# Kernel tuning notes

Hardware: AMD Instinct MI355X
Metric: run time of the kernel (lower is better)

The kernel has to match this reference:

```python
import jax, jax.numpy as jnp
import numpy as np

N_NODES = 50000
N_EDGES = 640000
D_IN = 128
D_H = 128


def gcn_conv(x, edge_index_sl, W, b, n_nodes):
    # x: [N, d_in]; edge_index_sl: [2, E+N] (self-loops already appended)
    h = x @ W  # [N, d_out]
    row, col = edge_index_sl[0], edge_index_sl[1]
    deg = jax.ops.segment_sum(jnp.ones(row.shape[0], dtype=x.dtype), col,
                              num_segments=n_nodes)
    dis = jnp.where(deg > 0, jax.lax.rsqrt(jnp.maximum(deg, 1e-12)), 0.0)
    norm = dis[row] * dis[col]  # [E+N]
    msg = h[row] * norm[:, None]  # gather + scale, [E+N, d_out]
    out = jax.ops.segment_sum(msg, col, num_segments=n_nodes)  # scatter-add
    return out + b


def setup_inputs() -> dict:
    key = jax.random.key(0)
    ks = jax.random.split(key, 9)
    x = jax.random.normal(ks[0], (N_NODES, D_IN), dtype=jnp.float32)
    edge_index = jax.random.randint(ks[1], (2, N_EDGES), 0, N_NODES, dtype=jnp.int64)
    s0 = 1.0 / np.sqrt(D_IN)
    s1 = 1.0 / np.sqrt(D_H)
    W0 = jax.random.uniform(ks[2], (D_IN, D_H), jnp.float32, -s0, s0)
    b0 = jnp.zeros((D_H,), jnp.float32)
    W1 = jax.random.uniform(ks[3], (D_H, D_H), jnp.float32, -s1, s1)
    b1 = jnp.zeros((D_H,), jnp.float32)
    W2 = jax.random.uniform(ks[4], (D_H, D_H), jnp.float32, -s1, s1)
    b2 = jnp.zeros((D_H,), jnp.float32)
    return {"x": x, "edge_index": edge_index, "W0": W0, "b0": b0,
            "W1": W1, "b1": b1, "W2": W2, "b2": b2}


def reference(x, edge_index, W0, b0, W1, b1, W2, b2):
    n = x.shape[0]
    # GCNConv adds self-loops: append (i, i) for every node.
    loops = jnp.arange(n, dtype=edge_index.dtype)
    ei = jnp.concatenate([edge_index, jnp.stack([loops, loops])], axis=1)
    h = x
    for W, b in ((W0, b0), (W1, b1), (W2, b2)):
        h = gcn_conv(h, ei, W, b, n)
        h = jax.nn.relu(h)  # dropout is identity in eval mode
    return h
```

## Files before the change

kernel.cpp:

```cpp
#include <hip/hip_runtime.h>
#include <hip/hip_bf16.h>

#define D 128
#define CAP 64
typedef _Float16 f16;
typedef unsigned short u16;
typedef f16 f16x8 __attribute__((ext_vector_type(8)));
typedef f16 f16x2 __attribute__((ext_vector_type(2)));
typedef float f32x4 __attribute__((ext_vector_type(4)));



__global__ void scatter_cvt_kernel(const int* __restrict__ row, const int* __restrict__ col,
                                   int* __restrict__ fill, u16* __restrict__ ssrc, int E,
                                   const float* __restrict__ W0, const float* __restrict__ W1,
                                   const float* __restrict__ W2,
                                   const float* __restrict__ b0, const float* __restrict__ b1,
                                   const float* __restrict__ b2,
                                   f16* __restrict__ WT, float* __restrict__ bperm) {
    const int EB = (E + 255) >> 8;
    const int b = blockIdx.x;
    if (b < EB) {
        int i = b * 256 + threadIdx.x;
        if (i < E) {
            int d = col[i];
            int p = atomicAdd(&fill[d], 1);
            if (p < CAP) ssrc[(size_t)d * CAP + p] = (u16)row[i];
        }
    } else {
        int id = (b - EB) * 256 + threadIdx.x;
        if (id < 49152) {
            int l = id >> 14;
            int e = id & 16383;
            int j = e >> 7;
            int nn = e & 127;
            int k = (l == 0) ? j : ((j >> 3) + 16 * (j & 7));
            const float* W = (l == 0) ? W0 : (l == 1) ? W1 : W2;
            WT[(size_t)l * 16384 + nn * 128 + j] = (f16)W[k * 128 + nn];
        } else if (id < 49536) {
            int j = id - 49152;
            int l = j >> 7;
            int pos = j & 127;
            int c = 16 * (pos & 7) + (pos >> 3);
            const float* bb = (l == 0) ? b0 : (l == 1) ? b1 : b2;
            bperm[l * 128 + pos] = bb[c];
        }
    }
}


template <bool A_F32>
__global__ __launch_bounds__(256) void gemm_mfma(const void* __restrict__ Aptr,
                                                 const f16* __restrict__ WT,
                                                 const int* __restrict__ fill,
                                                 f16* __restrict__ H, int n) {
    __shared__ f16 sW[128 * 128];
    const int tid  = threadIdx.x;
    const int w    = tid >> 6, lane = tid & 63;
    const int q    = lane >> 4, c = lane & 15;
    const int row0 = blockIdx.x * 64;

    int arow = row0 + w * 16 + c;
    if (arow >= n) arow = n - 1;

    f16x8 afr[4];
    if (A_F32) {
        float4 x0[4], x1[4];
        #pragma unroll
        for (int t = 0; t < 4; ++t) {
            const float* src = (const float*)Aptr + (size_t)arow * D + (t * 4 + q) * 8;
            x0[t] = *(const float4*)src;
            x1[t] = *(const float4*)(src + 4);
        }
        #pragma unroll
        for (int t = 0; t < 4; ++t) {
            f16x8 h;
            h[0] = (f16)x0[t].x; h[1] = (f16)x0[t].y; h[2] = (f16)x0[t].z; h[3] = (f16)x0[t].w;
            h[4] = (f16)x1[t].x; h[5] = (f16)x1[t].y; h[6] = (f16)x1[t].z; h[7] = (f16)x1[t].w;
            afr[t] = h;
        }
    } else {
        #pragma unroll
        for (int t = 0; t < 4; ++t)
            afr[t] = *(const f16x8*)((const f16*)Aptr + (size_t)arow * D + (t * 4 + q) * 8);
    }

    #pragma unroll
    for (int i = 0; i < 8; ++i) {
        int f = i * 256 + tid;
        int r = f >> 4, b = f & 15;
        int u = (r << 4) | (b ^ (r & 15));
        *(f16x8*)&sW[u * 8] = *(const f16x8*)&WT[(size_t)r * D + b * 8];
    }
    __syncthreads();

    f32x4 acc[8];
    #pragma unroll
    for (int nt = 0; nt < 8; ++nt) acc[nt] = (f32x4)0.f;

    #pragma unroll
    for (int nt = 0; nt < 8; ++nt) {
        const int rn = nt * 16 + c;
        #pragma unroll
        for (int t = 0; t < 4; ++t) {
            f16x8 bfr = *(const f16x8*)&sW[(((rn << 4) | ((t * 4 + q) ^ c))) * 8];
            acc[nt] = __builtin_amdgcn_mfma_f32_16x16x32_f16(afr[t], bfr, acc[nt], 0, 0, 0);
        }
    }

    const int rbase = row0 + w * 16 + q * 4;
    int4 fv4 = *(const int4*)&fill[rbase];
    #pragma unroll
    for (int reg = 0; reg < 4; ++reg) {
        int grow = rbase + reg;
        if (grow < n) {
            int fv = (reg == 0) ? fv4.x : (reg == 1) ? fv4.y : (reg == 2) ? fv4.z : fv4.w;
            float dv = rsqrtf((float)(fv + 1));
            f16x8 hh;
            #pragma unroll
            for (int nt = 0; nt < 8; ++nt) hh[nt] = (f16)(acc[nt][reg] * dv);
            *(f16x8*)&H[(size_t)grow * D + c * 8] = hh;
        }
    }
}


template <bool LAST>
__global__ __launch_bounds__(256) void agg_kernel(const f16* __restrict__ H,
                                                  const int* __restrict__ fill,
                                                  const u16* __restrict__ ssrc,
                                                  const float* __restrict__ bperm,
                                                  float* __restrict__ out,
                                                  f16* __restrict__ act, int n) {
    const int v    = (blockIdx.x * 256 + threadIdx.x) >> 6;
    const int lane = threadIdx.x & 63;
    if (v >= n) return;
    const int fo = lane * 2;

    f16x2 hv = *(const f16x2*)&H[(size_t)v * D + fo];
    float ax = (float)hv[0], ay = (float)hv[1];

    const int truedeg = fill[v];
    int deg = truedeg > CAP ? CAP : truedeg;
    int e = v * CAP;
    const int e1 = e + deg;
    for (; e + 8 <= e1; e += 8) {
        int s0 = ssrc[e],     s1 = ssrc[e + 1], s2 = ssrc[e + 2], s3 = ssrc[e + 3];
        int s4 = ssrc[e + 4], s5 = ssrc[e + 5], s6 = ssrc[e + 6], s7 = ssrc[e + 7];
        f16x2 h0 = *(const f16x2*)&H[(size_t)s0 * D + fo];
        f16x2 h1 = *(const f16x2*)&H[(size_t)s1 * D + fo];
        f16x2 h2 = *(const f16x2*)&H[(size_t)s2 * D + fo];
        f16x2 h3 = *(const f16x2*)&H[(size_t)s3 * D + fo];
        f16x2 h4 = *(const f16x2*)&H[(size_t)s4 * D + fo];
        f16x2 h5 = *(const f16x2*)&H[(size_t)s5 * D + fo];
        f16x2 h6 = *(const f16x2*)&H[(size_t)s6 * D + fo];
        f16x2 h7 = *(const f16x2*)&H[(size_t)s7 * D + fo];
        float px = ((float)h0[0] + (float)h1[0]) + ((float)h2[0] + (float)h3[0]);
        float py = ((float)h0[1] + (float)h1[1]) + ((float)h2[1] + (float)h3[1]);
        float qx = ((float)h4[0] + (float)h5[0]) + ((float)h6[0] + (float)h7[0]);
        float qy = ((float)h4[1] + (float)h5[1]) + ((float)h6[1] + (float)h7[1]);
        ax += px + qx;
        ay += py + qy;
    }
    for (; e + 2 <= e1; e += 2) {
        int s0 = ssrc[e], s1 = ssrc[e + 1];
        f16x2 h0 = *(const f16x2*)&H[(size_t)s0 * D + fo];
        f16x2 h1 = *(const f16x2*)&H[(size_t)s1 * D + fo];
        ax += (float)h0[0] + (float)h1[0];
        ay += (float)h0[1] + (float)h1[1];
    }
    if (e < e1) {
        int s = ssrc[e];
        f16x2 h = *(const f16x2*)&H[(size_t)s * D + fo];
        ax += (float)h[0];
        ay += (float)h[1];
    }

    const float dv = rsqrtf((float)(truedeg + 1));
    float2 bb = *(const float2*)&bperm[fo];
    float rx = fmaxf(fmaf(dv, ax, bb.x), 0.f);
    float ry = fmaxf(fmaf(dv, ay, bb.y), 0.f);
    if (LAST) {
        const int col0 = 16 * ((2 * lane) & 7) + (lane >> 2);
        out[(size_t)v * D + col0]      = rx;
        out[(size_t)v * D + col0 + 16] = ry;
    } else {
        f16x2 res;
        res[0] = (f16)rx; res[1] = (f16)ry;
        *(f16x2*)&act[(size_t)v * D + fo] = res;
    }
}


extern "C" void kernel_launch(void* const* d_in, const int* in_sizes, int n_in,
                              void* d_out, int out_size, void* d_ws, size_t ws_size,
                              hipStream_t stream) {
    const float* x  = (const float*)d_in[0];
    const int*   ei = (const int*)d_in[1];
    const float* W0 = (const float*)d_in[2];
    const float* b0 = (const float*)d_in[3];
    const float* W1 = (const float*)d_in[4];
    const float* b1 = (const float*)d_in[5];
    const float* W2 = (const float*)d_in[6];
    const float* b2 = (const float*)d_in[7];
    float* out = (float*)d_out;

    const int n = in_sizes[0] / D;
    const int E = in_sizes[1] / 2;
    const int n_pad = (n + 63) & ~63;
    const int* row = ei;
    const int* col = ei + E;
    const int EB = (E + 255) / 256;

    char* w = (char*)d_ws;
    size_t o = 0;
    f16* hbuf = (f16*)(w + o); o += (size_t)n_pad * D * 2;
    f16* act  = (f16*)(w + o); o += (size_t)n_pad * D * 2;
    f16* WT   = (f16*)(w + o); o += (size_t)3 * 16384 * 2;
    o = (o + 63) & ~(size_t)63;
    float* bperm = (float*)(w + o); o += 3 * 128 * 4;
    int* fill = (int*)(w + o); o += (size_t)n_pad * 4;
    o = (o + 127) & ~(size_t)127;
    u16* ssrc = (u16*)(w + o);

    hipMemsetAsync(fill, 0, (size_t)n_pad * 4, stream);
    scatter_cvt_kernel<<<EB + 194, 256, 0, stream>>>(row, col, fill, ssrc, E,
                                                     W0, W1, W2, b0, b1, b2, WT, bperm);

    const int gblocks = (n + 63) / 64;
    const int ablocks = (n + 3) / 4;

    gemm_mfma<true><<<gblocks, 256, 0, stream>>>(x, WT, fill, hbuf, n);
    agg_kernel<false><<<ablocks, 256, 0, stream>>>(hbuf, fill, ssrc, bperm, out, act, n);
    gemm_mfma<false><<<gblocks, 256, 0, stream>>>(act, WT + 16384, fill, hbuf, n);
    agg_kernel<false><<<ablocks, 256, 0, stream>>>(hbuf, fill, ssrc, bperm + 128, out, act, n);
    gemm_mfma<false><<<gblocks, 256, 0, stream>>>(act, WT + 2 * 16384, fill, hbuf, n);
    agg_kernel<true><<<ablocks, 256, 0, stream>>>(hbuf, fill, ssrc, bperm + 256, out, act, n);
}
```

Baseline: 246.0 us.

## Overlap edge scatter with first-layer GEMM by deferring degree scaling

Splits the weight and bias conversion into its own small kernel. The edge bucketing scatter is then fused with the first-layer GEMM in one launch, so the scatter atomics and the MFMA matmul run concurrently in different blocks. Because the first GEMM can no longer read degrees, its output is left unscaled. The first aggregation instead applies the per-source degree normalisation with an extra gather of fill[s] and an rsqrt per edge. This saves one launch and the serial dependency, at the cost of more per-edge work in layer one's aggregation.

```diff
diff --git a/kernel.cpp b/kernel.cpp
--- a/kernel.cpp
+++ b/kernel.cpp
@@ -11,13 +11,118 @@
 
 
 
-__global__ void scatter_cvt_kernel(const int* __restrict__ row, const int* __restrict__ col,
-                                   int* __restrict__ fill, u16* __restrict__ ssrc, int E,
-                                   const float* __restrict__ W0, const float* __restrict__ W1,
-                                   const float* __restrict__ W2,
-                                   const float* __restrict__ b0, const float* __restrict__ b1,
-                                   const float* __restrict__ b2,
-                                   f16* __restrict__ WT, float* __restrict__ bperm) {
+__global__ void cvt_kernel(const float* __restrict__ W0, const float* __restrict__ W1,
+                           const float* __restrict__ W2,
+                           const float* __restrict__ b0, const float* __restrict__ b1,
+                           const float* __restrict__ b2,
+                           f16* __restrict__ WT, float* __restrict__ bperm) {
+    int id = blockIdx.x * 256 + threadIdx.x;
+    if (id < 49152) {
+        int l = id >> 14;
+        int e = id & 16383;
+        int j = e >> 7;
+        int nn = e & 127;
+        int k = (l == 0) ? j : ((j >> 3) + 16 * (j & 7));
+        const float* W = (l == 0) ? W0 : (l == 1) ? W1 : W2;
+        WT[(size_t)l * 16384 + nn * 128 + j] = (f16)W[k * 128 + nn];
+    } else if (id < 49536) {
+        int j = id - 49152;
+        int l = j >> 7;
+        int pos = j & 127;
+        int c = 16 * (pos & 7) + (pos >> 3);
+        const float* bb = (l == 0) ? b0 : (l == 1) ? b1 : b2;
+        bperm[l * 128 + pos] = bb[c];
+    }
+}
+
+
+template <bool A_F32, bool SCALE>
+__device__ __forceinline__ void gemm_body(const void* __restrict__ Aptr,
+                                          const f16* __restrict__ WT,
+                                          const int* __restrict__ fill,
+                                          f16* __restrict__ H, int n,
+                                          int block, f16* sW, int tid) {
+    const int w    = tid >> 6, lane = tid & 63;
+    const int q    = lane >> 4, c = lane & 15;
+    const int row0 = block * 64;
+
+    int arow = row0 + w * 16 + c;
+    if (arow >= n) arow = n - 1;
+
+    f16x8 afr[4];
+    if (A_F32) {
+        float4 x0[4], x1[4];
+        #pragma unroll
+        for (int t = 0; t < 4; ++t) {
+            const float* src = (const float*)Aptr + (size_t)arow * D + (t * 4 + q) * 8;
+            x0[t] = *(const float4*)src;
+            x1[t] = *(const float4*)(src + 4);
+        }
+        #pragma unroll
+        for (int t = 0; t < 4; ++t) {
+            f16x8 h;
+            h[0] = (f16)x0[t].x; h[1] = (f16)x0[t].y; h[2] = (f16)x0[t].z; h[3] = (f16)x0[t].w;
+            h[4] = (f16)x1[t].x; h[5] = (f16)x1[t].y; h[6] = (f16)x1[t].z; h[7] = (f16)x1[t].w;
+            afr[t] = h;
+        }
+    } else {
+        #pragma unroll
+        for (int t = 0; t < 4; ++t)
+            afr[t] = *(const f16x8*)((const f16*)Aptr + (size_t)arow * D + (t * 4 + q) * 8);
+    }
+
+    #pragma unroll
+    for (int i = 0; i < 8; ++i) {
+        int f = i * 256 + tid;
+        int r = f >> 4, b = f & 15;
+        int u = (r << 4) | (b ^ (r & 15));
+        *(f16x8*)&sW[u * 8] = *(const f16x8*)&WT[(size_t)r * D + b * 8];
+    }
+    __syncthreads();
+
+    f32x4 acc[8];
+    #pragma unroll
+    for (int nt = 0; nt < 8; ++nt) acc[nt] = (f32x4)0.f;
+
+    #pragma unroll
+    for (int nt = 0; nt < 8; ++nt) {
+        const int rn = nt * 16 + c;
+        #pragma unroll
+        for (int t = 0; t < 4; ++t) {
+            f16x8 bfr = *(const f16x8*)&sW[(((rn << 4) | ((t * 4 + q) ^ c))) * 8];
+            acc[nt] = __builtin_amdgcn_mfma_f32_16x16x32_f16(afr[t], bfr, acc[nt], 0, 0, 0);
+        }
+    }
+
+    const int rbase = row0 + w * 16 + q * 4;
+    int4 fv4 = make_int4(0, 0, 0, 0);
+    if (SCALE) fv4 = *(const int4*)&fill[rbase];
+    #pragma unroll
+    for (int reg = 0; reg < 4; ++reg) {
+        int grow = rbase + reg;
+        if (grow < n) {
+            f16x8 hh;
+            if (SCALE) {
+                int fv = (reg == 0) ? fv4.x : (reg == 1) ? fv4.y : (reg == 2) ? fv4.z : fv4.w;
+                float dv = rsqrtf((float)(fv + 1));
+                #pragma unroll
+                for (int nt = 0; nt < 8; ++nt) hh[nt] = (f16)(acc[nt][reg] * dv);
+            } else {
+                #pragma unroll
+                for (int nt = 0; nt < 8; ++nt) hh[nt] = (f16)acc[nt][reg];
+            }
+            *(f16x8*)&H[(size_t)grow * D + c * 8] = hh;
+        }
+    }
+}
+
+
+__global__ __launch_bounds__(256) void fused0_kernel(
+        const int* __restrict__ row, const int* __restrict__ col,
+        int* __restrict__ fill, u16* __restrict__ ssrc, int E,
+        const f16* __restrict__ WT,
+        const float* __restrict__ x, f16* __restrict__ H, int n) {
+    __shared__ f16 sW[128 * 128];
     const int EB = (E + 255) >> 8;
     const int b = blockIdx.x;
     if (b < EB) {
@@ -28,104 +133,20 @@
             if (p < CAP) ssrc[(size_t)d * CAP + p] = (u16)row[i];
         }
     } else {
-        int id = (b - EB) * 256 + threadIdx.x;
-        if (id < 49152) {
-            int l = id >> 14;
-            int e = id & 16383;
-            int j = e >> 7;
-            int nn = e & 127;
-            int k = (l == 0) ? j : ((j >> 3) + 16 * (j & 7));
-            const float* W = (l == 0) ? W0 : (l == 1) ? W1 : W2;
-            WT[(size_t)l * 16384 + nn * 128 + j] = (f16)W[k * 128 + nn];
-        } else if (id < 49536) {
-            int j = id - 49152;
-            int l = j >> 7;
-            int pos = j & 127;
-            int c = 16 * (pos & 7) + (pos >> 3);
-            const float* bb = (l == 0) ? b0 : (l == 1) ? b1 : b2;
-            bperm[l * 128 + pos] = bb[c];
-        }
-    }
-}
-
-
-template <bool A_F32>
-__global__ __launch_bounds__(256) void gemm_mfma(const void* __restrict__ Aptr,
+        gemm_body<true, false>(x, WT, fill, H, n, b - EB, sW, threadIdx.x);
+    }
+}
+
+__global__ __launch_bounds__(256) void gemm_mfma(const f16* __restrict__ Aptr,
                                                  const f16* __restrict__ WT,
                                                  const int* __restrict__ fill,
                                                  f16* __restrict__ H, int n) {
     __shared__ f16 sW[128 * 128];
-    const int tid  = threadIdx.x;
-    const int w    = tid >> 6, lane = tid & 63;
-    const int q    = lane >> 4, c = lane & 15;
-    const int row0 = blockIdx.x * 64;
-
-    int arow = row0 + w * 16 + c;
-    if (arow >= n) arow = n - 1;
-
-    f16x8 afr[4];
-    if (A_F32) {
-        float4 x0[4], x1[4];
-        #pragma unroll
-        for (int t = 0; t < 4; ++t) {
-            const float* src = (const float*)Aptr + (size_t)arow * D + (t * 4 + q) * 8;
-            x0[t] = *(const float4*)src;
-            x1[t] = *(const float4*)(src + 4);
-        }
-        #pragma unroll
-        for (int t = 0; t < 4; ++t) {
-            f16x8 h;
-            h[0] = (f16)x0[t].x; h[1] = (f16)x0[t].y; h[2] = (f16)x0[t].z; h[3] = (f16)x0[t].w;
-            h[4] = (f16)x1[t].x; h[5] = (f16)x1[t].y; h[6] = (f16)x1[t].z; h[7] = (f16)x1[t].w;
-            afr[t] = h;
-        }
-    } else {
-        #pragma unroll
-        for (int t = 0; t < 4; ++t)
-            afr[t] = *(const f16x8*)((const f16*)Aptr + (size_t)arow * D + (t * 4 + q) * 8);
-    }
-
-    #pragma unroll
-    for (int i = 0; i < 8; ++i) {
-        int f = i * 256 + tid;
-        int r = f >> 4, b = f & 15;
-        int u = (r << 4) | (b ^ (r & 15));
-        *(f16x8*)&sW[u * 8] = *(const f16x8*)&WT[(size_t)r * D + b * 8];
-    }
-    __syncthreads();
-
-    f32x4 acc[8];
-    #pragma unroll
-    for (int nt = 0; nt < 8; ++nt) acc[nt] = (f32x4)0.f;
-
-    #pragma unroll
-    for (int nt = 0; nt < 8; ++nt) {
-        const int rn = nt * 16 + c;
-        #pragma unroll
-        for (int t = 0; t < 4; ++t) {
-            f16x8 bfr = *(const f16x8*)&sW[(((rn << 4) | ((t * 4 + q) ^ c))) * 8];
-            acc[nt] = __builtin_amdgcn_mfma_f32_16x16x32_f16(afr[t], bfr, acc[nt], 0, 0, 0);
-        }
-    }
-
-    const int rbase = row0 + w * 16 + q * 4;
-    int4 fv4 = *(const int4*)&fill[rbase];
-    #pragma unroll
-    for (int reg = 0; reg < 4; ++reg) {
-        int grow = rbase + reg;
-        if (grow < n) {
-            int fv = (reg == 0) ? fv4.x : (reg == 1) ? fv4.y : (reg == 2) ? fv4.z : fv4.w;
-            float dv = rsqrtf((float)(fv + 1));
-            f16x8 hh;
-            #pragma unroll
-            for (int nt = 0; nt < 8; ++nt) hh[nt] = (f16)(acc[nt][reg] * dv);
-            *(f16x8*)&H[(size_t)grow * D + c * 8] = hh;
-        }
-    }
-}
-
-
-template <bool LAST>
+    gemm_body<false, true>(Aptr, WT, fill, H, n, blockIdx.x, sW, threadIdx.x);
+}
+
+
+template <bool SCALED, bool LAST>
 __global__ __launch_bounds__(256) void agg_kernel(const f16* __restrict__ H,
                                                   const int* __restrict__ fill,
                                                   const u16* __restrict__ ssrc,
@@ -137,10 +158,14 @@
     if (v >= n) return;
     const int fo = lane * 2;
 
+    const int truedeg = fill[v];
+    const float dv = rsqrtf((float)(truedeg + 1));
+
     f16x2 hv = *(const f16x2*)&H[(size_t)v * D + fo];
-    float ax = (float)hv[0], ay = (float)hv[1];
-
-    const int truedeg = fill[v];
+    float ax, ay;
+    if (SCALED) { ax = (float)hv[0];      ay = (float)hv[1]; }
+    else        { ax = dv * (float)hv[0]; ay = dv * (float)hv[1]; }
+
     int deg = truedeg > CAP ? CAP : truedeg;
     int e = v * CAP;
     const int e1 = e + deg;
@@ -155,28 +180,37 @@
         f16x2 h5 = *(const f16x2*)&H[(size_t)s5 * D + fo];
         f16x2 h6 = *(const f16x2*)&H[(size_t)s6 * D + fo];
         f16x2 h7 = *(const f16x2*)&H[(size_t)s7 * D + fo];
-        float px = ((float)h0[0] + (float)h1[0]) + ((float)h2[0] + (float)h3[0]);
-        float py = ((float)h0[1] + (float)h1[1]) + ((float)h2[1] + (float)h3[1]);
-        float qx = ((float)h4[0] + (float)h5[0]) + ((float)h6[0] + (float)h7[0]);
-        float qy = ((float)h4[1] + (float)h5[1]) + ((float)h6[1] + (float)h7[1]);
-        ax += px + qx;
-        ay += py + qy;
-    }
-    for (; e + 2 <= e1; e += 2) {
-        int s0 = ssrc[e], s1 = ssrc[e + 1];
-        f16x2 h0 = *(const f16x2*)&H[(size_t)s0 * D + fo];
-        f16x2 h1 = *(const f16x2*)&H[(size_t)s1 * D + fo];
-        ax += (float)h0[0] + (float)h1[0];
-        ay += (float)h0[1] + (float)h1[1];
-    }
-    if (e < e1) {
+        if (SCALED) {
+            float px = ((float)h0[0] + (float)h1[0]) + ((float)h2[0] + (float)h3[0]);
+            float py = ((float)h0[1] + (float)h1[1]) + ((float)h2[1] + (float)h3[1]);
+            float qx = ((float)h4[0] + (float)h5[0]) + ((float)h6[0] + (float)h7[0]);
+            float qy = ((float)h4[1] + (float)h5[1]) + ((float)h6[1] + (float)h7[1]);
+            ax += px + qx;
+            ay += py + qy;
+        } else {
+            float w0 = rsqrtf((float)(fill[s0] + 1)), w1 = rsqrtf((float)(fill[s1] + 1));
+            float w2 = rsqrtf((float)(fill[s2] + 1)), w3 = rsqrtf((float)(fill[s3] + 1));
+            float w4 = rsqrtf((float)(fill[s4] + 1)), w5 = rsqrtf((float)(fill[s5] + 1));
+            float w6 = rsqrtf((float)(fill[s6] + 1)), w7 = rsqrtf((float)(fill[s7] + 1));
+            ax += w0*(float)h0[0] + w1*(float)h1[0] + w2*(float)h2[0] + w3*(float)h3[0]
+                + w4*(float)h4[0] + w5*(float)h5[0] + w6*(float)h6[0] + w7*(float)h7[0];
+            ay += w0*(float)h0[1] + w1*(float)h1[1] + w2*(float)h2[1] + w3*(float)h3[1]
+                + w4*(float)h4[1] + w5*(float)h5[1] + w6*(float)h6[1] + w7*(float)h7[1];
+        }
+    }
+    for (; e < e1; ++e) {
         int s = ssrc[e];
         f16x2 h = *(const f16x2*)&H[(size_t)s * D + fo];
-        ax += (float)h[0];
-        ay += (float)h[1];
-    }
-
-    const float dv = rsqrtf((float)(truedeg + 1));
+        if (SCALED) {
+            ax += (float)h[0];
+            ay += (float)h[1];
+        } else {
+            float ws = rsqrtf((float)(fill[s] + 1));
+            ax += ws * (float)h[0];
+            ay += ws * (float)h[1];
+        }
+    }
+
     float2 bb = *(const float2*)&bperm[fo];
     float rx = fmaxf(fmaf(dv, ax, bb.x), 0.f);
     float ry = fmaxf(fmaf(dv, ay, bb.y), 0.f);
@@ -223,17 +257,15 @@
     o = (o + 127) & ~(size_t)127;
     u16* ssrc = (u16*)(w + o);
 
-    hipMemsetAsync(fill, 0, (size_t)n_pad * 4, stream);
-    scatter_cvt_kernel<<<EB + 194, 256, 0, stream>>>(row, col, fill, ssrc, E,
-                                                     W0, W1, W2, b0, b1, b2, WT, bperm);
-
     const int gblocks = (n + 63) / 64;
     const int ablocks = (n + 3) / 4;
 
-    gemm_mfma<true><<<gblocks, 256, 0, stream>>>(x, WT, fill, hbuf, n);
-    agg_kernel<false><<<ablocks, 256, 0, stream>>>(hbuf, fill, ssrc, bperm, out, act, n);
-    gemm_mfma<false><<<gblocks, 256, 0, stream>>>(act, WT + 16384, fill, hbuf, n);
-    agg_kernel<false><<<ablocks, 256, 0, stream>>>(hbuf, fill, ssrc, bperm + 128, out, act, n);
-    gemm_mfma<false><<<gblocks, 256, 0, stream>>>(act, WT + 2 * 16384, fill, hbuf, n);
-    agg_kernel<true><<<ablocks, 256, 0, stream>>>(hbuf, fill, ssrc, bperm + 256, out, act, n);
-}
+    hipMemsetAsync(fill, 0, (size_t)n_pad * 4, stream);
+    cvt_kernel<<<194, 256, 0, stream>>>(W0, W1, W2, b0, b1, b2, WT, bperm);
+    fused0_kernel<<<EB + gblocks, 256, 0, stream>>>(row, col, fill, ssrc, E, WT, x, hbuf, n);
+    agg_kernel<false, false><<<ablocks, 256, 0, stream>>>(hbuf, fill, ssrc, bperm, out, act, n);
+    gemm_mfma<<<gblocks, 256, 0, stream>>>(act, WT + 16384, fill, hbuf, n);
+    agg_kernel<true, false><<<ablocks, 256, 0, stream>>>(hbuf, fill, ssrc, bperm + 128, out, act, n);
+    gemm_mfma<<<gblocks, 256, 0, stream>>>(act, WT + 2 * 16384, fill, hbuf, n);
+    agg_kernel<true, true><<<ablocks, 256, 0, stream>>>(hbuf, fill, ssrc, bperm + 256, out, act, n);
+}
```

Result: slower. 274.7 us (+11.7%).
